# Kernel optimization log

Measured on AMD Instinct MI355X. Metric: run time of the kernel, lower is better.

## Reference

```python
import jax, jax.numpy as jnp
import numpy as np

EPS = 1e-3  # Keras LayerNormalization default epsilon


def layernorm(x, g, b):
    mu = jnp.mean(x, axis=-1, keepdims=True)
    var = jnp.var(x, axis=-1, keepdims=True)
    return (x - mu) * jax.lax.rsqrt(var + EPS) * g + b


def setup_inputs() -> dict:
    key = jax.random.key(0)
    ks = jax.random.split(key, 16)
    B, T, C = 2, 2048, 1024
    F = 4 * C
    std = 0.02
    inp = {
        "x": jax.random.normal(ks[0], (B, T, C), jnp.float32),
        "ln1_g": jnp.ones((C,), jnp.float32),
        "ln1_b": jnp.zeros((C,), jnp.float32),
        "Wq": std * jax.random.normal(ks[1], (C, C), jnp.float32),
        "bq": jnp.zeros((C,), jnp.float32),
        "Wk": std * jax.random.normal(ks[2], (C, C), jnp.float32),
        "bk": jnp.zeros((C,), jnp.float32),
        "Wv": std * jax.random.normal(ks[3], (C, C), jnp.float32),
        "bv": jnp.zeros((C,), jnp.float32),
        "ln2_g": jnp.ones((C,), jnp.float32),
        "ln2_b": jnp.zeros((C,), jnp.float32),
        "W1": std * jax.random.normal(ks[4], (C, F), jnp.float32),
        "b1": jnp.zeros((F,), jnp.float32),
        "W2": std * jax.random.normal(ks[5], (F, C), jnp.float32),
        "b2": jnp.zeros((C,), jnp.float32),
    }
    return inp


N_HEADS = 16


def reference(x, ln1_g, ln1_b, Wq, bq, Wk, bk, Wv, bv, ln2_g, ln2_b, W1, b1, W2, b2):
    B, T, C = x.shape
    H = N_HEADS
    D = C // H

    h = layernorm(x, ln1_g, ln1_b)
    # [B,T,C] -> [B,H,T,D]
    def split_heads(y):
        return y.reshape(B, T, H, D).transpose(0, 2, 1, 3)

    q = split_heads(h @ Wq + bq)
    k = split_heads(h @ Wk + bk)
    v = split_heads(h @ Wv + bv)

    # Faithful to original: scores = K @ Q^T, i.e. scores[i,j] = k_i . q_j
    scores = jnp.einsum("bhid,bhjd->bhij", k, q) / jnp.sqrt(jnp.float32(D))
    causal = jnp.tril(jnp.ones((T, T), bool))  # [T,T]
    scores = jnp.where(causal[None, None], scores, -jnp.inf)
    w = jax.nn.softmax(scores, axis=-1)
    attn = jnp.einsum("bhij,bhjd->bhid", w, v)  # [B,H,T,D]
    attn = attn.transpose(0, 2, 1, 3).reshape(B, T, C)
    x = x + attn

    h2 = layernorm(x, ln2_g, ln2_b)
    ffn = jax.nn.gelu(h2 @ W1 + b1, approximate=False) @ W2 + b2
    x = x + ffn
    return x
```

## Files before the change

### kernel.cpp

```cpp
#include <hip/hip_runtime.h>
#include <hip/hip_bf16.h>
#include <math.h>

typedef __hip_bfloat16 bf16;
typedef __attribute__((ext_vector_type(8))) short bf16x8;
typedef __attribute__((ext_vector_type(4))) float f32x4;

__device__ __forceinline__ unsigned short f2bf_rne(float f) {
  unsigned u = __float_as_uint(f);
  u += 0x7fffu + ((u >> 16) & 1u);
  return (unsigned short)(u >> 16);
}
__device__ __forceinline__ float bf2f(unsigned short s) {
  return __uint_as_float(((unsigned)s) << 16);
}

__device__ __forceinline__ float gelu_fast(float v) {
  float u = v * (0.7978845608f + 0.0356774081f * v * v);
  float t = __builtin_amdgcn_exp2f(u * 2.8853900818f);
  float r = __builtin_amdgcn_rcpf(t + 1.0f);
  return v - v * r;
}

#define GLOBAL_AS __attribute__((address_space(1)))
#define LDS_AS __attribute__((address_space(3)))
__device__ __forceinline__ void gl2lds16(const void* g, void* l) {
  __builtin_amdgcn_global_load_lds((const GLOBAL_AS void*)g, (LDS_AS void*)l, 16, 0, 0);
}

__global__ __launch_bounds__(256) void ln_kernel(const float* __restrict__ x,
                                                 const float* __restrict__ g,
                                                 const float* __restrict__ b,
                                                 bf16* __restrict__ h) {
  int row = blockIdx.x, t = threadIdx.x;
  const float4 xv = ((const float4*)(x + (size_t)row * 1024))[t];
  float s = xv.x + xv.y + xv.z + xv.w;
  float sq = xv.x * xv.x + xv.y * xv.y + xv.z * xv.z + xv.w * xv.w;
  #pragma unroll
  for (int m = 1; m < 64; m <<= 1) { s += __shfl_xor(s, m); sq += __shfl_xor(sq, m); }
  __shared__ float ps[4], pq[4];
  if ((t & 63) == 0) { ps[t >> 6] = s; pq[t >> 6] = sq; }
  __syncthreads();
  s = ps[0] + ps[1] + ps[2] + ps[3];
  sq = pq[0] + pq[1] + pq[2] + pq[3];
  float mean = s * (1.0f / 1024.0f);
  float var = sq * (1.0f / 1024.0f) - mean * mean;
  float rs = rsqrtf(var + 1e-3f);
  float4 gv = ((const float4*)g)[t];
  float4 bv = ((const float4*)b)[t];
  ushort4 o;
  o.x = f2bf_rne((xv.x - mean) * rs * gv.x + bv.x);
  o.y = f2bf_rne((xv.y - mean) * rs * gv.y + bv.y);
  o.z = f2bf_rne((xv.z - mean) * rs * gv.z + bv.z);
  o.w = f2bf_rne((xv.w - mean) * rs * gv.w + bv.w);
  ((ushort4*)(h + (size_t)row * 1024))[t] = o;
}

__device__ __forceinline__ void tr_tile(const float* __restrict__ W, bf16* __restrict__ WT,
                                        int R, int Cc, int bx, int by, int t) {
  __shared__ float tile[32][33];
  int tx = t & 31, ty = t >> 5;
  #pragma unroll
  for (int k = 0; k < 4; k++) {
    int rr = ty + k * 8;
    tile[rr][tx] = W[(size_t)(by + rr) * Cc + bx + tx];
  }
  __syncthreads();
  unsigned short* out = reinterpret_cast<unsigned short*>(WT);
  #pragma unroll
  for (int k = 0; k < 4; k++) {
    int rr = ty + k * 8;
    out[(size_t)(bx + rr) * R + by + tx] = f2bf_rne(tile[tx][rr]);
  }
}

__global__ __launch_bounds__(256) void transpose_all(const float* __restrict__ Wq,
                                                     const float* __restrict__ Wk,
                                                     const float* __restrict__ Wv,
                                                     const float* __restrict__ W1,
                                                     const float* __restrict__ W2,
                                                     bf16* __restrict__ WqkT,
                                                     bf16* __restrict__ W1T,
                                                     bf16* __restrict__ W2T) {
  int id = blockIdx.x, t = threadIdx.x;
  if (id < 3072) {
    int sect = id >> 10, r = id & 1023;
    const float* W = sect == 0 ? Wq : (sect == 1 ? Wk : Wv);
    bf16* WT = WqkT + (size_t)sect * 1048576;
    tr_tile(W, WT, 1024, 1024, (r & 31) * 32, (r >> 5) * 32, t);
  } else if (id < 7168) {
    int r = id - 3072;
    tr_tile(W1, W1T, 1024, 4096, (r & 127) * 32, (r >> 7) * 32, t);
  } else {
    int r = id - 7168;
    tr_tile(W2, W2T, 4096, 1024, (r & 31) * 32, (r >> 5) * 32, t);
  }
}

__device__ __forceinline__ void kloop_bk64(const bf16* __restrict__ A,
                                           const bf16* __restrict__ BT,
                                           int K, int kbeg, int kend, int m0, int n0,
                                           int wave, int lane,
                                           bf16 (*As)[64], bf16 (*Bs)[64],
                                           f32x4 acc[4][4]) {
  int lrow = lane & 15, quad = lane >> 4;
  int wm = (wave >> 1) * 64, wn = (wave & 1) * 64;
  int srow = wave * 32 + (lane >> 3);
  int gsw = ((lane & 7) ^ (lane >> 3)) * 8;
  int sw = lrow & 7;
  for (int k0 = kbeg; k0 < kend; k0 += 64) {
    __syncthreads();
    #pragma unroll
    for (int j = 0; j < 4; j++) {
      int row = srow + j * 8;
      gl2lds16(A + (size_t)(m0 + row) * K + k0 + gsw, (char*)As + wave * 4096 + j * 1024);
      gl2lds16(BT + (size_t)(n0 + row) * K + k0 + gsw, (char*)Bs + wave * 4096 + j * 1024);
    }
    __syncthreads();
    bf16x8 af[2][4], bfr[2][4];
    #pragma unroll
    for (int h = 0; h < 2; h++) {
      #pragma unroll
      for (int i = 0; i < 4; i++)
        af[h][i] = *(const bf16x8*)((const char*)&As[wm + i * 16 + lrow][0] +
                                    (((h * 4 + quad) ^ sw) * 16));
      #pragma unroll
      for (int j = 0; j < 4; j++)
        bfr[h][j] = *(const bf16x8*)((const char*)&Bs[wn + j * 16 + lrow][0] +
                                     (((h * 4 + quad) ^ sw) * 16));
    }
    #pragma unroll
    for (int h = 0; h < 2; h++)
      #pragma unroll
      for (int i = 0; i < 4; i++)
        #pragma unroll
        for (int j = 0; j < 4; j++)
          acc[i][j] = __builtin_amdgcn_mfma_f32_16x16x32_bf16(af[h][i], bfr[h][j], acc[i][j], 0, 0, 0);
  }
}

__global__ __launch_bounds__(256) void gemm_ffn1(const bf16* __restrict__ A,
                                                 const bf16* __restrict__ BT,
                                                 const float* __restrict__ bias,
                                                 bf16* __restrict__ out,
                                                 int N, int K) {
  __shared__ bf16 As[128][64];
  __shared__ bf16 Bs[128][64];
  int t = threadIdx.x;
  int n0 = blockIdx.x * 128, m0 = blockIdx.y * 128;
  int lane = t & 63, wave = t >> 6;
  f32x4 acc[4][4];
  #pragma unroll
  for (int i = 0; i < 4; i++)
    #pragma unroll
    for (int j = 0; j < 4; j++) acc[i][j] = (f32x4){0.f, 0.f, 0.f, 0.f};
  kloop_bk64(A, BT, K, 0, K, m0, n0, wave, lane, As, Bs, acc);

  int wm = (wave >> 1) * 64, wn = (wave & 1) * 64;
  int r4 = (lane >> 4) * 4, cl = lane & 15;
  unsigned short* os = reinterpret_cast<unsigned short*>(out);
  #pragma unroll
  for (int i = 0; i < 4; i++)
    #pragma unroll
    for (int j = 0; j < 4; j++) {
      int col = n0 + wn + j * 16 + cl;
      float bval = bias[col];
      #pragma unroll
      for (int r = 0; r < 4; r++) {
        int row = m0 + wm + i * 16 + r4 + r;
        os[(size_t)row * N + col] = f2bf_rne(gelu_fast(acc[i][j][r] + bval));
      }
    }
}

__global__ __launch_bounds__(256) void gemm_ffn2_sk(const bf16* __restrict__ A,
                                                    const bf16* __restrict__ BT,
                                                    unsigned short* __restrict__ p0,
                                                    unsigned short* __restrict__ p1,
                                                    int K) {
  __shared__ bf16 As[128][64];
  __shared__ bf16 Bs[128][64];
  int t = threadIdx.x;
  int n0 = blockIdx.x * 128, m0 = blockIdx.y * 128;
  int z = blockIdx.z;
  int lane = t & 63, wave = t >> 6;
  f32x4 acc[4][4];
  #pragma unroll
  for (int i = 0; i < 4; i++)
    #pragma unroll
    for (int j = 0; j < 4; j++) acc[i][j] = (f32x4){0.f, 0.f, 0.f, 0.f};
  kloop_bk64(A, BT, K, z * 2048, z * 2048 + 2048, m0, n0, wave, lane, As, Bs, acc);

  unsigned short* p = z ? p1 : p0;
  int wm = (wave >> 1) * 64, wn = (wave & 1) * 64;
  int r4 = (lane >> 4) * 4, cl = lane & 15;
  #pragma unroll
  for (int i = 0; i < 4; i++)
    #pragma unroll
    for (int j = 0; j < 4; j++) {
      int col = n0 + wn + j * 16 + cl;
      #pragma unroll
      for (int r = 0; r < 4; r++) {
        int row = m0 + wm + i * 16 + r4 + r;
        p[(size_t)row * 1024 + col] = f2bf_rne(acc[i][j][r]);
      }
    }
}

__global__ __launch_bounds__(256) void reduce_ffn2(const unsigned short* __restrict__ p0,
                                                   const unsigned short* __restrict__ p1,
                                                   const float* __restrict__ x1,
                                                   const float* __restrict__ bias,
                                                   float* __restrict__ out) {
  int row = blockIdx.x, t = threadIdx.x;
  size_t base = (size_t)row * 1024;
  ushort4 a = ((const ushort4*)(p0 + base))[t];
  ushort4 b = ((const ushort4*)(p1 + base))[t];
  float4 xv = ((const float4*)(x1 + base))[t];
  float4 bv = ((const float4*)bias)[t];
  float4 o;
  o.x = bf2f(a.x) + bf2f(b.x) + xv.x + bv.x;
  o.y = bf2f(a.y) + bf2f(b.y) + xv.y + bv.y;
  o.z = bf2f(a.z) + bf2f(b.z) + xv.z + bv.z;
  o.w = bf2f(a.w) + bf2f(b.w) + xv.w + bv.w;
  ((float4*)(out + base))[t] = o;
}

__global__ __launch_bounds__(256) void gemm_qkv(const bf16* __restrict__ A,
                                                const bf16* __restrict__ BT,
                                                const float* __restrict__ bq,
                                                const float* __restrict__ bk,
                                                const float* __restrict__ bv,
                                                bf16* __restrict__ qb,
                                                bf16* __restrict__ kb,
                                                bf16* __restrict__ vt,
                                                int K) {
  __shared__ bf16 As[128][64];
  __shared__ bf16 Bs[128][64];
  int t = threadIdx.x;
  int n0 = blockIdx.x * 128, m0 = blockIdx.y * 128;
  int lane = t & 63, wave = t >> 6;
  f32x4 acc[4][4];
  #pragma unroll
  for (int i = 0; i < 4; i++)
    #pragma unroll
    for (int j = 0; j < 4; j++) acc[i][j] = (f32x4){0.f, 0.f, 0.f, 0.f};
  kloop_bk64(A, BT, K, 0, K, m0, n0, wave, lane, As, Bs, acc);

  int sect = n0 >> 10;
  const float* bias = sect == 0 ? bq : (sect == 1 ? bk : bv);
  int wm = (wave >> 1) * 64, wn = (wave & 1) * 64;
  int r4 = (lane >> 4) * 4, cl = lane & 15;
  #pragma unroll
  for (int i = 0; i < 4; i++)
    #pragma unroll
    for (int j = 0; j < 4; j++) {
      int col = n0 + wn + j * 16 + cl;
      int c1 = col & 1023;
      float bval = bias[c1];
      int row0 = m0 + wm + i * 16 + r4;
      if (sect < 2) {
        bf16* o = sect == 0 ? qb : kb;
        unsigned short* os = reinterpret_cast<unsigned short*>(o);
        #pragma unroll
        for (int r = 0; r < 4; r++)
          os[(size_t)(row0 + r) * 1024 + c1] = f2bf_rne(acc[i][j][r] + bval);
      } else {
        int hh = c1 >> 6, d = c1 & 63;
        int b = row0 >> 11, t0 = row0 & 2047;
        ushort4 pk;
        pk.x = f2bf_rne(acc[i][j][0] + bval);
        pk.y = f2bf_rne(acc[i][j][1] + bval);
        pk.z = f2bf_rne(acc[i][j][2] + bval);
        pk.w = f2bf_rne(acc[i][j][3] + bval);
        *(ushort4*)((unsigned short*)vt + (size_t)((b * 16 + hh) * 64 + d) * 2048 + t0) = pk;
      }
    }
}

__global__ __launch_bounds__(256) void attn_mfma(const bf16* __restrict__ qb,
                                                 const bf16* __restrict__ kb,
                                                 const bf16* __restrict__ vt,
                                                 const float* __restrict__ x,
                                                 float* __restrict__ x1) {
  __shared__ bf16 Qe[64][72];
  __shared__ bf16 Ke[64][72];
  __shared__ bf16 Vt[64][72];
  __shared__ bf16 Pls[64][72];
  int t = threadIdx.x;
  int bh = blockIdx.x;
  int b = bh >> 4, h = bh & 15;
  size_t qk_base = (size_t)b * 2048 * 1024 + (size_t)h * 64;
  size_t vt_base = (size_t)bh * 64 * 2048;
  int lane = t & 63, wave = t >> 6;
  int l = lane & 15, quad = lane >> 4;
  const float cs = 0.125f * 1.44269504088896f;

  for (int pass = 0; pass < 2; pass++) {
    int it = pass ? (31 - (int)blockIdx.y) : (int)blockIdx.y;
    int i0 = it * 64;
    __syncthreads();
    #pragma unroll
    for (int c0 = 0; c0 < 512; c0 += 256) {
      int c = c0 + t;
      int row = c >> 3, col8 = (c & 7) * 8;
      *(uint4*)&Qe[row][col8] = *(const uint4*)(kb + qk_base + (size_t)(i0 + row) * 1024 + col8);
    }
    __syncthreads();
    bf16x8 aq0 = *(const bf16x8*)&Qe[wave * 16 + l][quad * 8];
    bf16x8 aq1 = *(const bf16x8*)&Qe[wave * 16 + l][32 + quad * 8];

    float l_r[4] = {0.f, 0.f, 0.f, 0.f};
    f32x4 Oacc[4];
    #pragma unroll
    for (int dt = 0; dt < 4; dt++) Oacc[dt] = (f32x4){0.f, 0.f, 0.f, 0.f};

    for (int jt = 0; jt <= it; jt++) {
      int j0 = jt * 64;
      __syncthreads();
      #pragma unroll
      for (int c0 = 0; c0 < 512; c0 += 256) {
        int c = c0 + t;
        int row = c >> 3, col8 = (c & 7) * 8;
        *(uint4*)&Ke[row][col8] = *(const uint4*)(qb + qk_base + (size_t)(j0 + row) * 1024 + col8);
        *(uint4*)&Vt[row][col8] = *(const uint4*)(vt + vt_base + (size_t)row * 2048 + j0 + col8);
      }
      __syncthreads();

      f32x4 S[4];
      #pragma unroll
      for (int nt = 0; nt < 4; nt++) {
        bf16x8 bk0 = *(const bf16x8*)&Ke[nt * 16 + l][quad * 8];
        bf16x8 bk1 = *(const bf16x8*)&Ke[nt * 16 + l][32 + quad * 8];
        f32x4 s = (f32x4){0.f, 0.f, 0.f, 0.f};
        s = __builtin_amdgcn_mfma_f32_16x16x32_bf16(aq0, bk0, s, 0, 0, 0);
        s = __builtin_amdgcn_mfma_f32_16x16x32_bf16(aq1, bk1, s, 0, 0, 0);
        S[nt] = s;
      }
      if (jt == it) {
        #pragma unroll
        for (int nt = 0; nt < 4; nt++)
          #pragma unroll
          for (int r = 0; r < 4; r++)
            if (nt * 16 + l > wave * 16 + quad * 4 + r) S[nt][r] = -3.0e38f;
      }
      #pragma unroll
      for (int nt = 0; nt < 4; nt++) {
        float p0 = __builtin_amdgcn_exp2f(S[nt][0] * cs);
        float p1 = __builtin_amdgcn_exp2f(S[nt][1] * cs);
        float p2 = __builtin_amdgcn_exp2f(S[nt][2] * cs);
        float p3 = __builtin_amdgcn_exp2f(S[nt][3] * cs);
        l_r[0] += p0; l_r[1] += p1; l_r[2] += p2; l_r[3] += p3;
        unsigned short* pr = (unsigned short*)&Pls[wave * 16 + quad * 4][nt * 16 + l];
        pr[0] = f2bf_rne(p0);
        pr[72] = f2bf_rne(p1);
        pr[144] = f2bf_rne(p2);
        pr[216] = f2bf_rne(p3);
      }
      asm volatile("s_waitcnt lgkmcnt(0)" ::: "memory");
      bf16x8 ap0 = *(const bf16x8*)&Pls[wave * 16 + l][quad * 8];
      bf16x8 ap1 = *(const bf16x8*)&Pls[wave * 16 + l][32 + quad * 8];
      #pragma unroll
      for (int dt = 0; dt < 4; dt++) {
        bf16x8 bv0 = *(const bf16x8*)&Vt[dt * 16 + l][quad * 8];
        bf16x8 bv1 = *(const bf16x8*)&Vt[dt * 16 + l][32 + quad * 8];
        Oacc[dt] = __builtin_amdgcn_mfma_f32_16x16x32_bf16(ap0, bv0, Oacc[dt], 0, 0, 0);
        Oacc[dt] = __builtin_amdgcn_mfma_f32_16x16x32_bf16(ap1, bv1, Oacc[dt], 0, 0, 0);
      }
    }

    #pragma unroll
    for (int r = 0; r < 4; r++) {
      float v = l_r[r];
      v += __shfl_xor(v, 1); v += __shfl_xor(v, 2);
      v += __shfl_xor(v, 4); v += __shfl_xor(v, 8);
      l_r[r] = v;
    }
    #pragma unroll
    for (int r = 0; r < 4; r++) {
      float inv = 1.0f / l_r[r];
      int row = i0 + wave * 16 + quad * 4 + r;
      size_t gi = qk_base + (size_t)row * 1024;
      #pragma unroll
      for (int dt = 0; dt < 4; dt++) {
        int d = dt * 16 + l;
        x1[gi + d] = x[gi + d] + Oacc[dt][r] * inv;
      }
    }
  }
}

extern "C" void kernel_launch(void* const* d_in, const int* in_sizes, int n_in,
                              void* d_out, int out_size, void* d_ws, size_t ws_size,
                              hipStream_t stream) {
  const float* x    = (const float*)d_in[0];
  const float* ln1g = (const float*)d_in[1];
  const float* ln1b = (const float*)d_in[2];
  const float* Wq   = (const float*)d_in[3];
  const float* bq   = (const float*)d_in[4];
  const float* Wk   = (const float*)d_in[5];
  const float* bk   = (const float*)d_in[6];
  const float* Wv   = (const float*)d_in[7];
  const float* bv   = (const float*)d_in[8];
  const float* ln2g = (const float*)d_in[9];
  const float* ln2b = (const float*)d_in[10];
  const float* W1   = (const float*)d_in[11];
  const float* b1   = (const float*)d_in[12];
  const float* W2   = (const float*)d_in[13];
  const float* b2   = (const float*)d_in[14];

  char* ws = (char*)d_ws;
  float* x1  = (float*)(ws + 0);
  bf16* h    = (bf16*)(ws + 16777216);
  bf16* WqkT = (bf16*)(ws + 25165824);
  bf16* W1T  = (bf16*)(ws + 31457280);
  bf16* W2T  = (bf16*)(ws + 39845888);
  bf16* qb   = (bf16*)(ws + 48234496);
  bf16* kb   = (bf16*)(ws + 56623104);
  bf16* vt   = (bf16*)(ws + 65011712);
  bf16* act  = (bf16*)(ws + 73400320);

  transpose_all<<<11264, 256, 0, stream>>>(Wq, Wk, Wv, W1, W2, WqkT, W1T, W2T);
  ln_kernel<<<4096, 256, 0, stream>>>(x, ln1g, ln1b, h);
  gemm_qkv<<<dim3(24, 32), 256, 0, stream>>>(h, WqkT, bq, bk, bv, qb, kb, vt, 1024);
  attn_mfma<<<dim3(32, 16), 256, 0, stream>>>(qb, kb, vt, x, x1);
  ln_kernel<<<4096, 256, 0, stream>>>(x1, ln2g, ln2b, h);
  gemm_ffn1<<<dim3(32, 32), 256, 0, stream>>>(h, W1T, b1, act, 4096, 1024);
  gemm_ffn2_sk<<<dim3(8, 32, 2), 256, 0, stream>>>(act, W2T,
      (unsigned short*)qb, (unsigned short*)kb, 4096);
  reduce_ffn2<<<4096, 256, 0, stream>>>((const unsigned short*)qb, (const unsigned short*)kb,
                                        x1, b2, (float*)d_out);
}
```

Measured before the change: 339.6 us.

## Enlarge attention query tile to 128 rows with two sub-tiles per wave

The attention kernel now processes 128 query rows per block, with each wave handling two 16-row sub-tiles, so every K/V tile loaded into shared memory feeds twice as many MFMAs. The score MFMA operands are swapped so P is produced row-major and written as packed ushort4. The causal mask moves from a separate last-tile pass into a per-element predicate. The grid halves to 256 blocks, which lowers parallelism on a many-CU GPU, and the diagonal tiles now do more masked work.

```diff
diff --git a/kernel.cpp b/kernel.cpp
--- a/kernel.cpp
+++ b/kernel.cpp
@@ -283,10 +283,10 @@
                                                  const bf16* __restrict__ vt,
                                                  const float* __restrict__ x,
                                                  float* __restrict__ x1) {
-  __shared__ bf16 Qe[64][72];
+  __shared__ bf16 Qe[128][72];
   __shared__ bf16 Ke[64][72];
   __shared__ bf16 Vt[64][72];
-  __shared__ bf16 Pls[64][72];
+  __shared__ bf16 Pls[128][72];
   int t = threadIdx.x;
   int bh = blockIdx.x;
   int b = bh >> 4, h = bh & 15;
@@ -297,94 +297,106 @@
   const float cs = 0.125f * 1.44269504088896f;
 
   for (int pass = 0; pass < 2; pass++) {
-    int it = pass ? (31 - (int)blockIdx.y) : (int)blockIdx.y;
-    int i0 = it * 64;
+    int it = pass ? (15 - (int)blockIdx.y) : (int)blockIdx.y;
+    int i0 = it * 128;
     __syncthreads();
     #pragma unroll
-    for (int c0 = 0; c0 < 512; c0 += 256) {
+    for (int c0 = 0; c0 < 1024; c0 += 256) {
       int c = c0 + t;
       int row = c >> 3, col8 = (c & 7) * 8;
       *(uint4*)&Qe[row][col8] = *(const uint4*)(kb + qk_base + (size_t)(i0 + row) * 1024 + col8);
     }
     __syncthreads();
-    bf16x8 aq0 = *(const bf16x8*)&Qe[wave * 16 + l][quad * 8];
-    bf16x8 aq1 = *(const bf16x8*)&Qe[wave * 16 + l][32 + quad * 8];
-
-    float l_r[4] = {0.f, 0.f, 0.f, 0.f};
-    f32x4 Oacc[4];
-    #pragma unroll
-    for (int dt = 0; dt < 4; dt++) Oacc[dt] = (f32x4){0.f, 0.f, 0.f, 0.f};
-
-    for (int jt = 0; jt <= it; jt++) {
-      int j0 = jt * 64;
+    bf16x8 qf[2][2];
+    #pragma unroll
+    for (int s = 0; s < 2; s++) {
+      int ib = (wave * 2 + s) * 16;
+      qf[s][0] = *(const bf16x8*)&Qe[ib + l][quad * 8];
+      qf[s][1] = *(const bf16x8*)&Qe[ib + l][32 + quad * 8];
+    }
+    float lsum[2] = {0.f, 0.f};
+    f32x4 Oacc[2][4];
+    #pragma unroll
+    for (int s = 0; s < 2; s++)
+      #pragma unroll
+      for (int dt = 0; dt < 4; dt++) Oacc[s][dt] = (f32x4){0.f, 0.f, 0.f, 0.f};
+
+    int njt = 2 * it + 2;
+    for (int jt = 0; jt < njt; jt++) {
+      int j0v = jt * 64;
       __syncthreads();
       #pragma unroll
       for (int c0 = 0; c0 < 512; c0 += 256) {
         int c = c0 + t;
         int row = c >> 3, col8 = (c & 7) * 8;
-        *(uint4*)&Ke[row][col8] = *(const uint4*)(qb + qk_base + (size_t)(j0 + row) * 1024 + col8);
-        *(uint4*)&Vt[row][col8] = *(const uint4*)(vt + vt_base + (size_t)row * 2048 + j0 + col8);
+        *(uint4*)&Ke[row][col8] = *(const uint4*)(qb + qk_base + (size_t)(j0v + row) * 1024 + col8);
+        *(uint4*)&Vt[row][col8] = *(const uint4*)(vt + vt_base + (size_t)row * 2048 + j0v + col8);
       }
       __syncthreads();
 
-      f32x4 S[4];
       #pragma unroll
       for (int nt = 0; nt < 4; nt++) {
-        bf16x8 bk0 = *(const bf16x8*)&Ke[nt * 16 + l][quad * 8];
-        bf16x8 bk1 = *(const bf16x8*)&Ke[nt * 16 + l][32 + quad * 8];
-        f32x4 s = (f32x4){0.f, 0.f, 0.f, 0.f};
-        s = __builtin_amdgcn_mfma_f32_16x16x32_bf16(aq0, bk0, s, 0, 0, 0);
-        s = __builtin_amdgcn_mfma_f32_16x16x32_bf16(aq1, bk1, s, 0, 0, 0);
-        S[nt] = s;
-      }
-      if (jt == it) {
+        bf16x8 kf0 = *(const bf16x8*)&Ke[nt * 16 + l][quad * 8];
+        bf16x8 kf1 = *(const bf16x8*)&Ke[nt * 16 + l][32 + quad * 8];
         #pragma unroll
-        for (int nt = 0; nt < 4; nt++)
-          #pragma unroll
-          for (int r = 0; r < 4; r++)
-            if (nt * 16 + l > wave * 16 + quad * 4 + r) S[nt][r] = -3.0e38f;
-      }
-      #pragma unroll
-      for (int nt = 0; nt < 4; nt++) {
-        float p0 = __builtin_amdgcn_exp2f(S[nt][0] * cs);
-        float p1 = __builtin_amdgcn_exp2f(S[nt][1] * cs);
-        float p2 = __builtin_amdgcn_exp2f(S[nt][2] * cs);
-        float p3 = __builtin_amdgcn_exp2f(S[nt][3] * cs);
-        l_r[0] += p0; l_r[1] += p1; l_r[2] += p2; l_r[3] += p3;
-        unsigned short* pr = (unsigned short*)&Pls[wave * 16 + quad * 4][nt * 16 + l];
-        pr[0] = f2bf_rne(p0);
-        pr[72] = f2bf_rne(p1);
-        pr[144] = f2bf_rne(p2);
-        pr[216] = f2bf_rne(p3);
+        for (int s = 0; s < 2; s++) {
+          int i_ = i0 + (wave * 2 + s) * 16 + l;
+          int jbase = j0v + nt * 16 + quad * 4;
+          f32x4 sv = (f32x4){0.f, 0.f, 0.f, 0.f};
+          sv = __builtin_amdgcn_mfma_f32_16x16x32_bf16(kf0, qf[s][0], sv, 0, 0, 0);
+          sv = __builtin_amdgcn_mfma_f32_16x16x32_bf16(kf1, qf[s][1], sv, 0, 0, 0);
+          ushort4 pk;
+          float p;
+          p = (jbase + 0 > i_) ? 0.f : __builtin_amdgcn_exp2f(sv[0] * cs);
+          lsum[s] += p; pk.x = f2bf_rne(p);
+          p = (jbase + 1 > i_) ? 0.f : __builtin_amdgcn_exp2f(sv[1] * cs);
+          lsum[s] += p; pk.y = f2bf_rne(p);
+          p = (jbase + 2 > i_) ? 0.f : __builtin_amdgcn_exp2f(sv[2] * cs);
+          lsum[s] += p; pk.z = f2bf_rne(p);
+          p = (jbase + 3 > i_) ? 0.f : __builtin_amdgcn_exp2f(sv[3] * cs);
+          lsum[s] += p; pk.w = f2bf_rne(p);
+          *(ushort4*)&Pls[(wave * 2 + s) * 16 + l][nt * 16 + quad * 4] = pk;
+        }
       }
       asm volatile("s_waitcnt lgkmcnt(0)" ::: "memory");
-      bf16x8 ap0 = *(const bf16x8*)&Pls[wave * 16 + l][quad * 8];
-      bf16x8 ap1 = *(const bf16x8*)&Pls[wave * 16 + l][32 + quad * 8];
+
+      bf16x8 ap[2][2];
+      #pragma unroll
+      for (int s = 0; s < 2; s++) {
+        int rowp = (wave * 2 + s) * 16 + l;
+        ap[s][0] = *(const bf16x8*)&Pls[rowp][quad * 8];
+        ap[s][1] = *(const bf16x8*)&Pls[rowp][32 + quad * 8];
+      }
       #pragma unroll
       for (int dt = 0; dt < 4; dt++) {
         bf16x8 bv0 = *(const bf16x8*)&Vt[dt * 16 + l][quad * 8];
         bf16x8 bv1 = *(const bf16x8*)&Vt[dt * 16 + l][32 + quad * 8];
-        Oacc[dt] = __builtin_amdgcn_mfma_f32_16x16x32_bf16(ap0, bv0, Oacc[dt], 0, 0, 0);
-        Oacc[dt] = __builtin_amdgcn_mfma_f32_16x16x32_bf16(ap1, bv1, Oacc[dt], 0, 0, 0);
-      }
-    }
-
-    #pragma unroll
-    for (int r = 0; r < 4; r++) {
-      float v = l_r[r];
-      v += __shfl_xor(v, 1); v += __shfl_xor(v, 2);
-      v += __shfl_xor(v, 4); v += __shfl_xor(v, 8);
-      l_r[r] = v;
-    }
-    #pragma unroll
-    for (int r = 0; r < 4; r++) {
-      float inv = 1.0f / l_r[r];
-      int row = i0 + wave * 16 + quad * 4 + r;
-      size_t gi = qk_base + (size_t)row * 1024;
-      #pragma unroll
-      for (int dt = 0; dt < 4; dt++) {
-        int d = dt * 16 + l;
-        x1[gi + d] = x[gi + d] + Oacc[dt][r] * inv;
+        #pragma unroll
+        for (int s = 0; s < 2; s++) {
+          Oacc[s][dt] = __builtin_amdgcn_mfma_f32_16x16x32_bf16(ap[s][0], bv0, Oacc[s][dt], 0, 0, 0);
+          Oacc[s][dt] = __builtin_amdgcn_mfma_f32_16x16x32_bf16(ap[s][1], bv1, Oacc[s][dt], 0, 0, 0);
+        }
+      }
+    }
+
+    #pragma unroll
+    for (int s = 0; s < 2; s++) {
+      lsum[s] += __shfl_xor(lsum[s], 16);
+      lsum[s] += __shfl_xor(lsum[s], 32);
+    }
+    #pragma unroll
+    for (int s = 0; s < 2; s++) {
+      #pragma unroll
+      for (int r = 0; r < 4; r++) {
+        float lv = __shfl(lsum[s], quad * 4 + r);
+        float inv = 1.0f / lv;
+        int row = i0 + (wave * 2 + s) * 16 + quad * 4 + r;
+        size_t gi = qk_base + (size_t)row * 1024;
+        #pragma unroll
+        for (int dt = 0; dt < 4; dt++) {
+          int d = dt * 16 + l;
+          x1[gi + d] = x[gi + d] + Oacc[s][dt][r] * inv;
+        }
       }
     }
   }
@@ -423,7 +435,7 @@
   transpose_all<<<11264, 256, 0, stream>>>(Wq, Wk, Wv, W1, W2, WqkT, W1T, W2T);
   ln_kernel<<<4096, 256, 0, stream>>>(x, ln1g, ln1b, h);
   gemm_qkv<<<dim3(24, 32), 256, 0, stream>>>(h, WqkT, bq, bk, bv, qb, kb, vt, 1024);
-  attn_mfma<<<dim3(32, 16), 256, 0, stream>>>(qb, kb, vt, x, x1);
+  attn_mfma<<<dim3(32, 8), 256, 0, stream>>>(qb, kb, vt, x, x1);
   ln_kernel<<<4096, 256, 0, stream>>>(x1, ln2g, ln2b, h);
   gemm_ffn1<<<dim3(32, 32), 256, 0, stream>>>(h, W1T, b1, act, 4096, 1024);
   gemm_ffn2_sk<<<dim3(8, 32, 2), 256, 0, stream>>>(act, W2T,
```

After: 333.3 us. About the same (-1.8%).
